# Kernel tuning notes

Hardware: AMD Instinct MI355X
Metric: run time of the kernel (lower is better)

## Reference

```python
import jax, jax.numpy as jnp
import numpy as np

N_NODES = 100000
N_EDGES = 1600000
IN_DIM = 128
HIDDEN = 128
N_GRAPHS = 256


def setup_inputs() -> dict:
    key = jax.random.key(0)
    ks = jax.random.split(key, 12)
    x = jax.random.normal(ks[0], (N_NODES, IN_DIM), dtype=jnp.float32)
    edge_index = jax.random.randint(ks[1], (2, N_EDGES), 0, N_NODES, dtype=jnp.int64)
    batch = jnp.sort(jax.random.randint(ks[2], (N_NODES,), 0, N_GRAPHS, dtype=jnp.int64))
    s = 0.05
    W1 = jax.random.normal(ks[3], (IN_DIM, HIDDEN), dtype=jnp.float32) * s
    b1 = jnp.zeros((HIDDEN,), dtype=jnp.float32)
    W2 = jax.random.normal(ks[4], (HIDDEN, HIDDEN), dtype=jnp.float32) * s
    b2 = jnp.zeros((HIDDEN,), dtype=jnp.float32)
    W3 = jax.random.normal(ks[5], (HIDDEN, HIDDEN), dtype=jnp.float32) * s
    b3 = jnp.zeros((HIDDEN,), dtype=jnp.float32)
    Wh = jax.random.normal(ks[6], (HIDDEN, 2), dtype=jnp.float32) * s
    bh = jnp.zeros((2,), dtype=jnp.float32)
    return {"x": x, "edge_index": edge_index, "batch": batch,
            "W1": W1, "b1": b1, "W2": W2, "b2": b2, "W3": W3, "b3": b3,
            "Wh": Wh, "bh": bh}


def _gcn_structure(edge_index, n_nodes):
    # PyG GCNConv default: add self-loops, symmetric deg^-1/2 normalization.
    loop = jnp.arange(n_nodes, dtype=edge_index.dtype)
    src = jnp.concatenate([edge_index[0], loop])  # message source j
    dst = jnp.concatenate([edge_index[1], loop])  # aggregate at i
    deg = jax.ops.segment_sum(jnp.ones_like(dst, dtype=jnp.float32), dst,
                              num_segments=n_nodes)
    dinv = jnp.where(deg > 0, jax.lax.rsqrt(deg), 0.0)
    norm = dinv[src] * dinv[dst]  # [E + N]
    return src, dst, norm


def _gcn_conv(x, W, b, src, dst, norm, n_nodes):
    h = x @ W  # dense transform first (PyG order)
    msg = h[src] * norm[:, None]  # gather + per-edge scale
    agg = jax.ops.segment_sum(msg, dst, num_segments=n_nodes)  # scatter-add
    return agg + b


def reference(x, edge_index, batch, W1, b1, W2, b2, W3, b3, Wh, bh):
    n = x.shape[0]
    src, dst, norm = _gcn_structure(edge_index, n)
    # dropout is a no-op in eval mode (training=False)
    h = jax.nn.relu(_gcn_conv(x, W1, b1, src, dst, norm, n))
    h = jax.nn.relu(_gcn_conv(h, W2, b2, src, dst, norm, n))
    h = jax.nn.relu(_gcn_conv(h, W3, b3, src, dst, norm, n))
    # global_mean_pool over graph ids
    sums = jax.ops.segment_sum(h, batch, num_segments=N_GRAPHS)
    cnts = jax.ops.segment_sum(jnp.ones((n,), dtype=h.dtype), batch,
                               num_segments=N_GRAPHS)
    pooled = sums / jnp.maximum(cnts, 1.0)[:, None]
    return pooled @ Wh + bh  # [N_GRAPHS, 2]
```

## Files before the change

kernel.cpp:

```cpp
#include <hip/hip_runtime.h>


#define D 128
#define NB_SHIFT 8
#define BCAP 8192
#define EPB 4096

typedef unsigned int uint;
typedef unsigned short ushort;
typedef __attribute__((ext_vector_type(8))) short short8;
typedef __attribute__((ext_vector_type(4))) float f32x4;

__device__ __forceinline__ ushort f2bf(float f) {
    uint u = __float_as_uint(f);
    uint r = (u + 0x7fffu + ((u >> 16) & 1u)) >> 16;
    return (ushort)r;
}
__device__ __forceinline__ float bf2f(ushort b) {
    return __uint_as_float(((uint)b) << 16);
}
__device__ __forceinline__ float q15f(uint q) {
    return __uint_as_float(0x30000000u | (q << 13));
}

__device__ __forceinline__ void async_cp16(const ushort* g, ushort* lds_uniform) {
    __builtin_amdgcn_global_load_lds(
        (const __attribute__((address_space(1))) unsigned int*)g,
        (__attribute__((address_space(3))) unsigned int*)lds_uniform,
        16, 0, 0);
}

__device__ __forceinline__ void bucketA_body(const int* __restrict__ src,
                                             const int* __restrict__ dst, int E,
                                             int nbk, int* __restrict__ gcur,
                                             uint* __restrict__ arena, int bid,
                                             int* hist, int* rbase) {
    int t = threadIdx.x;
    int e0 = bid * EPB;
    int e1 = min(e0 + EPB, E);
    for (int i = t; i < nbk; i += 256) hist[i] = 0;
    __syncthreads();
    for (int e = e0 + t; e < e1; e += 256)
        atomicAdd(&hist[dst[e] >> NB_SHIFT], 1);
    __syncthreads();
    for (int i = t; i < nbk; i += 256) {
        int c = hist[i];
        rbase[i] = (c > 0) ? atomicAdd(&gcur[i], c) : 0;
        hist[i] = 0;
    }
    __syncthreads();
    for (int e = e0 + t; e < e1; e += 256) {
        int d = dst[e];
        int s = src[e];
        int b = d >> NB_SHIFT;
        int pos = rbase[b] + atomicAdd(&hist[b], 1);
        if (pos < BCAP)
            arena[(size_t)b * BCAP + pos] =
                ((uint)(d & ((1 << NB_SHIFT) - 1)) << 17) | (uint)s;
    }
}

template <bool AF32>
__device__ __forceinline__ void gemm_body(const void* __restrict__ Ain,
                                          const ushort* __restrict__ Wf,
                                          ushort* __restrict__ out, int N,
                                          int rowb, ushort* As) {
    int t = threadIdx.x;

    if (AF32) {
        const float* A = (const float*)Ain;
#pragma unroll
        for (int i = 0; i < 8; i++) {
            int u = i * 256 + t;
            int row = u >> 5, c4 = u & 31;
            int grow = rowb + row;
            float4 v = make_float4(0.f, 0.f, 0.f, 0.f);
            if (grow < N) v = *(const float4*)(A + (size_t)grow * D + c4 * 4);
            uint2 p;
            p.x = (uint)f2bf(v.x) | ((uint)f2bf(v.y) << 16);
            p.y = (uint)f2bf(v.z) | ((uint)f2bf(v.w) << 16);
            int byteoff = row * 256 + ((c4 * 8) ^ ((row & 7) << 4));
            *(uint2*)((char*)As + byteoff) = p;
        }
    } else {
        const ushort* A = (const ushort*)Ain;
#pragma unroll
        for (int i = 0; i < 4; i++) {
            int u = i * 256 + t;
            int row = u >> 4, cp = u & 15;
            int grow = rowb + row;
            if (grow >= N) grow = N - 1;
            int gc = cp ^ (row & 7);
            const ushort* gp = A + (size_t)grow * D + gc * 8;
            ushort* lb = As + (size_t)(i * 256 + (t & 192)) * 8;
            async_cp16(gp, lb);
        }
        asm volatile("s_waitcnt vmcnt(0)" ::: "memory");
    }
    __syncthreads();

    int wave = t >> 6, lane = t & 63;
    const short8* Wf8 = (const short8*)Wf;

    short8 bhi[2][4], blo[2][4];
#pragma unroll
    for (int j = 0; j < 2; j++) {
        int nt = wave * 2 + j;
#pragma unroll
        for (int kt = 0; kt < 4; kt++) {
            bhi[j][kt] = Wf8[(size_t)((0 * 4 + kt) * 8 + nt) * 64 + lane];
            blo[j][kt] = Wf8[(size_t)((1 * 4 + kt) * 8 + nt) * 64 + lane];
        }
    }

    f32x4 acc[4][2];
#pragma unroll
    for (int m = 0; m < 4; m++)
#pragma unroll
        for (int j = 0; j < 2; j++) acc[m][j] = (f32x4){0.f, 0.f, 0.f, 0.f};

#pragma unroll
    for (int m = 0; m < 4; m++) {
        int r = m * 16 + (lane & 15);
#pragma unroll
        for (int kt = 0; kt < 4; kt++) {
            int raw = kt * 64 + (lane >> 4) * 16;
            short8 a = *(const short8*)((const char*)As + r * 256 + (raw ^ ((r & 7) << 4)));
#pragma unroll
            for (int j = 0; j < 2; j++) {
                acc[m][j] = __builtin_amdgcn_mfma_f32_16x16x32_bf16(a, bhi[j][kt], acc[m][j], 0, 0, 0);
                acc[m][j] = __builtin_amdgcn_mfma_f32_16x16x32_bf16(a, blo[j][kt], acc[m][j], 0, 0, 0);
            }
        }
    }

#pragma unroll
    for (int m = 0; m < 4; m++) {
#pragma unroll
        for (int j = 0; j < 2; j++) {
            int colb = (wave * 2 + j) * 16 + (lane & 15);
#pragma unroll
            for (int jj = 0; jj < 4; jj++) {
                int grow = rowb + m * 16 + (lane >> 4) * 4 + jj;
                if (grow < N)
                    out[(size_t)grow * D + colb] = f2bf(acc[m][j][jj]);
            }
        }
    }
}

__global__ __launch_bounds__(256) void k_build_gemm1(const int* __restrict__ src,
                                                     const int* __restrict__ dst, int E,
                                                     int nbk, int* __restrict__ gcur,
                                                     uint* __restrict__ arena, int nA,
                                                     const float* __restrict__ x,
                                                     const ushort* __restrict__ Wf,
                                                     ushort* __restrict__ T, int N) {
    __shared__ ushort As[64 * D];
    if ((int)blockIdx.x < nA) {
        int* hist = (int*)As;
        int* rbase = hist + 512;
        bucketA_body(src, dst, E, nbk, gcur, arena, blockIdx.x, hist, rbase);
    } else {
        gemm_body<true>(x, Wf, T, N, (blockIdx.x - nA) * 64, As);
    }
}

template <bool AF32>
__global__ __launch_bounds__(256) void k_gemm(const void* __restrict__ Ain,
                                              const ushort* __restrict__ Wf,
                                              ushort* __restrict__ out, int N) {
    __shared__ ushort As[64 * D];
    gemm_body<AF32>(Ain, Wf, out, N, blockIdx.x * 64, As);
}

__global__ void k_scanG(const int* __restrict__ gcur, int nbk, int E,
                        int* __restrict__ bbase, int* __restrict__ row_start, int N) {
    __shared__ int s[512];
    int t = threadIdx.x;
    s[t] = (t < nbk) ? gcur[t] : 0;
    __syncthreads();
    for (int off = 1; off < 512; off <<= 1) {
        int x = (t >= off) ? s[t - off] : 0;
        __syncthreads();
        s[t] += x;
        __syncthreads();
    }
    if (t < nbk) bbase[t] = s[t] - gcur[t];
    if (t == 0) row_start[N] = E;
}

__global__ __launch_bounds__(256) void k_degB2(const uint* __restrict__ arena,
                                               const int* __restrict__ gcur,
                                               const int* __restrict__ bbase, int N,
                                               float* __restrict__ dinv,
                                               int* __restrict__ row_start) {
    int b = blockIdx.x;
    int t = threadIdx.x;
    __shared__ int hist[256];
    __shared__ int sc[256];
    hist[t] = 0;
    __syncthreads();
    int cnt = min(gcur[b], BCAP);
    const uint* seg = arena + (size_t)b * BCAP;
    for (int i = t; i < cnt; i += 256)
        atomicAdd(&hist[seg[i] >> 17], 1);
    __syncthreads();
    int c = hist[t];
    sc[t] = c;
    __syncthreads();
    for (int off = 1; off < 256; off <<= 1) {
        int x = (t >= off) ? sc[t - off] : 0;
        __syncthreads();
        sc[t] += x;
        __syncthreads();
    }
    int node = (b << NB_SHIFT) + t;
    if (node < N) {
        dinv[node] = rsqrtf((float)(c + 1));
        row_start[node] = bbase[b] + sc[t] - c;
    }
}

__global__ __launch_bounds__(256) void k_bucketB(const uint* __restrict__ arena,
                                                 const int* __restrict__ gcur,
                                                 const int* __restrict__ row_start,
                                                 const float* __restrict__ dinv,
                                                 int N, uint* __restrict__ csr) {
    int b = blockIdx.x;
    int t = threadIdx.x;
    int n0 = b << NB_SHIFT;
    int nn = min(1 << NB_SHIFT, N - n0);
    __shared__ float sdinv[256];
    __shared__ int sstart[256];
    __shared__ int scur[256];
    __shared__ uint sout[BCAP];
    for (int i = t; i < nn; i += 256) {
        sdinv[i]  = dinv[n0 + i];
        sstart[i] = row_start[n0 + i];
        scur[i]   = 0;
    }
    __syncthreads();
    int cnt = min(gcur[b], BCAP);
    int csr0 = sstart[0];
    for (int i = t; i < cnt; i += 256) {
        uint en = arena[(size_t)b * BCAP + i];
        int dl = en >> 17;
        int s  = en & 0x1FFFF;
        float nrm = dinv[s] * sdinv[dl];
        uint q = ((__float_as_uint(nrm) + 0x1000u) >> 13) & 0x7FFFu;
        int pos = atomicAdd(&scur[dl], 1);
        sout[(sstart[dl] - csr0) + pos] = ((uint)s << 15) | q;
    }
    __syncthreads();
    for (int i = t; i < cnt; i += 256)
        csr[csr0 + i] = sout[i];
}

__global__ void k_wsplit3(const float* __restrict__ W1, const float* __restrict__ W2,
                          const float* __restrict__ W3, ushort* __restrict__ Wf) {
    int gidx = blockIdx.x * blockDim.x + threadIdx.x;
    if (gidx >= 3 * 32768) return;
    int which = gidx >> 15;
    int idx = gidx & 32767;
    const float* W = (which == 0) ? W1 : (which == 1) ? W2 : W3;
    int i  = idx & 7;
    int l  = (idx >> 3) & 63;
    int nt = (idx >> 9) & 7;
    int kt = (idx >> 12) & 3;
    int h  = idx >> 14;
    int k = kt * 32 + (l >> 4) * 8 + i;
    int n = nt * 16 + (l & 15);
    float w = W[k * D + n];
    ushort hi = f2bf(w);
    ushort v = (h == 0) ? hi : f2bf(w - bf2f(hi));
    Wf[gidx] = v;
}

__device__ __forceinline__ void agg_core(const ushort* __restrict__ T,
                                         const uint* __restrict__ csr,
                                         int beg, int end, int col,
                                         float& a0, float& a1) {
    if (beg >= end) return;
    int lane16 = threadIdx.x & 15;
    uint cur = csr[min(beg + lane16, end - 1)];
    for (int e = beg; e < end; e += 16) {
        uint nxt = 0;
        int en = e + 16;
        if (en < end) nxt = csr[min(en + lane16, end - 1)];
        uint v[16];
        float nn[16];
#pragma unroll
        for (int q = 0; q < 16; q++) {
            uint c = __builtin_amdgcn_readlane(cur, q);
            nn[q] = (e + q < end) ? q15f(c & 0x7FFFu) : 0.f;
            v[q] = *(const uint*)(T + (size_t)(c >> 15) * D + col);
        }
#pragma unroll
        for (int q = 0; q < 16; q++) {
            a0 = fmaf(nn[q], __uint_as_float(v[q] << 16), a0);
            a1 = fmaf(nn[q], __uint_as_float(v[q] & 0xffff0000u), a1);
        }
        cur = nxt;
    }
}

__global__ __launch_bounds__(256) void k_agg(const ushort* __restrict__ T,
                                             const float* __restrict__ dinv,
                                             const int* __restrict__ row_start,
                                             const uint* __restrict__ csr,
                                             const float* __restrict__ bias,
                                             ushort* __restrict__ out, int N) {
    int node = __builtin_amdgcn_readfirstlane(blockIdx.x * 4 + (threadIdx.x >> 6));
    if (node >= N) return;
    int lane = threadIdx.x & 63;
    int col = lane * 2;

    float di = dinv[node];
    uint vs = *(const uint*)(T + (size_t)node * D + col);
    float sw = di * di;
    float a0 = sw * __uint_as_float(vs << 16);
    float a1 = sw * __uint_as_float(vs & 0xffff0000u);

    agg_core(T, csr, row_start[node], row_start[node + 1], col, a0, a1);

    a0 = fmaxf(a0 + bias[col], 0.f);
    a1 = fmaxf(a1 + bias[col + 1], 0.f);
    ushort2 o; o.x = f2bf(a0); o.y = f2bf(a1);
    *(ushort2*)(out + (size_t)node * D + col) = o;
}

__global__ __launch_bounds__(256) void k_agg_head(const ushort* __restrict__ T,
                                                  const float* __restrict__ dinv,
                                                  const int* __restrict__ row_start,
                                                  const uint* __restrict__ csr,
                                                  const float* __restrict__ bias,
                                                  const float* __restrict__ Wh,
                                                  float2* __restrict__ y, int N) {
    int node = __builtin_amdgcn_readfirstlane(blockIdx.x * 4 + (threadIdx.x >> 6));
    if (node >= N) return;
    int lane = threadIdx.x & 63;
    int col = lane * 2;

    float di = dinv[node];
    uint vs = *(const uint*)(T + (size_t)node * D + col);
    float sw = di * di;
    float a0 = sw * __uint_as_float(vs << 16);
    float a1 = sw * __uint_as_float(vs & 0xffff0000u);

    agg_core(T, csr, row_start[node], row_start[node + 1], col, a0, a1);

    a0 = fmaxf(a0 + bias[col], 0.f);
    a1 = fmaxf(a1 + bias[col + 1], 0.f);

    float p0 = a0 * Wh[col * 2 + 0] + a1 * Wh[(col + 1) * 2 + 0];
    float p1 = a0 * Wh[col * 2 + 1] + a1 * Wh[(col + 1) * 2 + 1];
#pragma unroll
    for (int off = 32; off > 0; off >>= 1) {
        p0 += __shfl_xor(p0, off);
        p1 += __shfl_xor(p1, off);
    }
    if (lane == 0) y[node] = make_float2(p0, p1);
}

__global__ __launch_bounds__(256) void k_pool2(const float2* __restrict__ y,
                                               const int* __restrict__ batch, int N,
                                               const float* __restrict__ bh,
                                               float* __restrict__ out) {
    int g = blockIdx.x;
    int t = threadIdx.x;
    int lo = 0, hi = N;
    while (lo < hi) { int m = (lo + hi) >> 1; if (batch[m] < g) lo = m + 1; else hi = m; }
    int beg = lo;
    lo = 0; hi = N;
    while (lo < hi) { int m = (lo + hi) >> 1; if (batch[m] < g + 1) lo = m + 1; else hi = m; }
    int endi = lo;

    float s0 = 0.f, s1 = 0.f;
    for (int i = beg + t; i < endi; i += 256) {
        float2 v = y[i];
        s0 += v.x; s1 += v.y;
    }
    __shared__ float r0[256], r1[256];
    r0[t] = s0; r1[t] = s1;
    __syncthreads();
    for (int off = 128; off > 0; off >>= 1) {
        if (t < off) { r0[t] += r0[t + off]; r1[t] += r1[t + off]; }
        __syncthreads();
    }
    if (t == 0) {
        float cnt = (float)((endi - beg) > 0 ? (endi - beg) : 1);
        out[g * 2 + 0] = r0[0] / cnt + bh[0];
        out[g * 2 + 1] = r1[0] / cnt + bh[1];
    }
}

extern "C" void kernel_launch(void* const* d_in, const int* in_sizes, int n_in,
                              void* d_out, int out_size, void* d_ws, size_t ws_size,
                              hipStream_t stream) {
    const float* x   = (const float*)d_in[0];
    const int* eidx  = (const int*)d_in[1];
    const int* batch = (const int*)d_in[2];
    const float* W1 = (const float*)d_in[3];
    const float* b1 = (const float*)d_in[4];
    const float* W2 = (const float*)d_in[5];
    const float* b2 = (const float*)d_in[6];
    const float* W3 = (const float*)d_in[7];
    const float* b3 = (const float*)d_in[8];
    const float* Wh = (const float*)d_in[9];
    const float* bh = (const float*)d_in[10];

    int E = in_sizes[1] / 2;
    int N = in_sizes[2];
    int ngraphs = out_size / 2;
    const int* src = eidx;
    const int* dst = eidx + E;
    int nbk = (N + (1 << NB_SHIFT) - 1) >> NB_SHIFT;

    char* ws = (char*)d_ws;
    size_t off = 0;
    auto alloc = [&](size_t bytes) -> void* {
        void* p = ws + off;
        off = (off + bytes + 255) & ~(size_t)255;
        return p;
    };
    ushort* Hbf      = (ushort*)alloc((size_t)N * D * 2);
    ushort* T        = (ushort*)alloc((size_t)N * D * 2);
    ushort* Wf       = (ushort*)alloc(3 * 32768 * 2);
    float*  dinv     = (float*)alloc((size_t)N * 4);
    int*    row_start= (int*)alloc((size_t)(N + 1) * 4);
    int*    gcur     = (int*)alloc((size_t)nbk * 4);
    int*    bbase    = (int*)alloc((size_t)nbk * 4);
    float2* y        = (float2*)alloc((size_t)N * 8);
    uint*   csr      = (uint*)alloc((size_t)E * 4);
    uint*   arena    = (uint*)alloc((size_t)nbk * BCAP * 4);
    (void)ws_size;

    hipMemsetAsync(gcur, 0, (size_t)nbk * 4, stream);
    k_wsplit3<<<384, 256, 0, stream>>>(W1, W2, W3, Wf);

    int gemm_grid = (N + 63) / 64;
    int agg_grid = (N + 3) / 4;
    int nA = (E + EPB - 1) / EPB;

    k_build_gemm1<<<nA + gemm_grid, 256, 0, stream>>>(src, dst, E, nbk, gcur, arena,
                                                      nA, x, Wf, T, N);
    k_scanG<<<1, 512, 0, stream>>>(gcur, nbk, E, bbase, row_start, N);
    k_degB2<<<nbk, 256, 0, stream>>>(arena, gcur, bbase, N, dinv, row_start);
    k_bucketB<<<nbk, 256, 0, stream>>>(arena, gcur, row_start, dinv, N, csr);

    k_agg<<<agg_grid, 256, 0, stream>>>(T, dinv, row_start, csr, b1, Hbf, N);
    k_gemm<false><<<gemm_grid, 256, 0, stream>>>(Hbf, Wf + 32768, T, N);
    k_agg<<<agg_grid, 256, 0, stream>>>(T, dinv, row_start, csr, b2, Hbf, N);
    k_gemm<false><<<gemm_grid, 256, 0, stream>>>(Hbf, Wf + 65536, T, N);
    k_agg_head<<<agg_grid, 256, 0, stream>>>(T, dinv, row_start, csr, b3, Wh, y, N);
    k_pool2<<<ngraphs, 256, 0, stream>>>(y, batch, N, bh, (float*)d_out);
}
```

Before: 289.2 us.

## Fuse CSR build into one kernel and compute edge norms on the fly

```diff
diff --git a/kernel.cpp b/kernel.cpp
--- a/kernel.cpp
+++ b/kernel.cpp
@@ -18,9 +18,6 @@
 }
 __device__ __forceinline__ float bf2f(ushort b) {
     return __uint_as_float(((uint)b) << 16);
-}
-__device__ __forceinline__ float q15f(uint q) {
-    return __uint_as_float(0x30000000u | (q << 13));
 }
 
 __device__ __forceinline__ void async_cp16(const ushort* g, ushort* lds_uniform) {
@@ -174,92 +171,72 @@
     gemm_body<AF32>(Ain, Wf, out, N, blockIdx.x * 64, As);
 }
 
-__global__ void k_scanG(const int* __restrict__ gcur, int nbk, int E,
-                        int* __restrict__ bbase, int* __restrict__ row_start, int N) {
-    __shared__ int s[512];
-    int t = threadIdx.x;
-    s[t] = (t < nbk) ? gcur[t] : 0;
-    __syncthreads();
-    for (int off = 1; off < 512; off <<= 1) {
-        int x = (t >= off) ? s[t - off] : 0;
-        __syncthreads();
-        s[t] += x;
-        __syncthreads();
-    }
-    if (t < nbk) bbase[t] = s[t] - gcur[t];
-    if (t == 0) row_start[N] = E;
-}
-
-__global__ __launch_bounds__(256) void k_degB2(const uint* __restrict__ arena,
-                                               const int* __restrict__ gcur,
-                                               const int* __restrict__ bbase, int N,
-                                               float* __restrict__ dinv,
-                                               int* __restrict__ row_start) {
+__global__ __launch_bounds__(256) void k_bucketB2(const uint* __restrict__ arena,
+                                                  const int* __restrict__ gcur,
+                                                  int nbk, int N, int E,
+                                                  float* __restrict__ dinv,
+                                                  int* __restrict__ row_start,
+                                                  uint* __restrict__ csr) {
     int b = blockIdx.x;
     int t = threadIdx.x;
     __shared__ int hist[256];
     __shared__ int sc[256];
+    __shared__ uint sout[BCAP];
     hist[t] = 0;
     __syncthreads();
     int cnt = min(gcur[b], BCAP);
     const uint* seg = arena + (size_t)b * BCAP;
     for (int i = t; i < cnt; i += 256)
         atomicAdd(&hist[seg[i] >> 17], 1);
-    __syncthreads();
+
+    int p = 0;
+    if (t < b) p += gcur[t];
+    if (t + 256 < b) p += gcur[t + 256];
+    ((int*)sout)[t] = p;
+    __syncthreads();
+    for (int off2 = 128; off2 > 0; off2 >>= 1) {
+        if (t < off2) ((int*)sout)[t] += ((int*)sout)[t + off2];
+        __syncthreads();
+    }
+    int bbase = ((int*)sout)[0];
+
     int c = hist[t];
     sc[t] = c;
     __syncthreads();
-    for (int off = 1; off < 256; off <<= 1) {
-        int x = (t >= off) ? sc[t - off] : 0;
+    for (int off2 = 1; off2 < 256; off2 <<= 1) {
+        int x = (t >= off2) ? sc[t - off2] : 0;
         __syncthreads();
         sc[t] += x;
         __syncthreads();
     }
+    int excl = sc[t] - c;
+
     int node = (b << NB_SHIFT) + t;
     if (node < N) {
         dinv[node] = rsqrtf((float)(c + 1));
-        row_start[node] = bbase[b] + sc[t] - c;
-    }
-}
-
-__global__ __launch_bounds__(256) void k_bucketB(const uint* __restrict__ arena,
-                                                 const int* __restrict__ gcur,
-                                                 const int* __restrict__ row_start,
-                                                 const float* __restrict__ dinv,
-                                                 int N, uint* __restrict__ csr) {
-    int b = blockIdx.x;
-    int t = threadIdx.x;
-    int n0 = b << NB_SHIFT;
-    int nn = min(1 << NB_SHIFT, N - n0);
-    __shared__ float sdinv[256];
-    __shared__ int sstart[256];
-    __shared__ int scur[256];
-    __shared__ uint sout[BCAP];
-    for (int i = t; i < nn; i += 256) {
-        sdinv[i]  = dinv[n0 + i];
-        sstart[i] = row_start[n0 + i];
-        scur[i]   = 0;
-    }
-    __syncthreads();
-    int cnt = min(gcur[b], BCAP);
-    int csr0 = sstart[0];
+        row_start[node] = bbase + excl;
+    }
+    if (b == 0 && t == 0) row_start[N] = E;
+
+    sc[t] = excl;
+    hist[t] = 0;
+    __syncthreads();
     for (int i = t; i < cnt; i += 256) {
-        uint en = arena[(size_t)b * BCAP + i];
+        uint en = seg[i];
         int dl = en >> 17;
-        int s  = en & 0x1FFFF;
-        float nrm = dinv[s] * sdinv[dl];
-        uint q = ((__float_as_uint(nrm) + 0x1000u) >> 13) & 0x7FFFu;
-        int pos = atomicAdd(&scur[dl], 1);
-        sout[(sstart[dl] - csr0) + pos] = ((uint)s << 15) | q;
+        int pos = atomicAdd(&hist[dl], 1);
+        sout[sc[dl] + pos] = en & 0x1FFFF;
     }
     __syncthreads();
     for (int i = t; i < cnt; i += 256)
-        csr[csr0 + i] = sout[i];
+        csr[bbase + i] = sout[i];
 }
 
 __global__ void k_wsplit3(const float* __restrict__ W1, const float* __restrict__ W2,
-                          const float* __restrict__ W3, ushort* __restrict__ Wf) {
+                          const float* __restrict__ W3, ushort* __restrict__ Wf,
+                          int* __restrict__ gcur, int nbk) {
     int gidx = blockIdx.x * blockDim.x + threadIdx.x;
+    if (gidx < nbk) gcur[gidx] = 0;
     if (gidx >= 3 * 32768) return;
     int which = gidx >> 15;
     int idx = gidx & 32767;
@@ -279,7 +256,8 @@
 
 __device__ __forceinline__ void agg_core(const ushort* __restrict__ T,
                                          const uint* __restrict__ csr,
-                                         int beg, int end, int col,
+                                         const float* __restrict__ dinv,
+                                         float di, int beg, int end, int col,
                                          float& a0, float& a1) {
     if (beg >= end) return;
     int lane16 = threadIdx.x & 15;
@@ -293,8 +271,9 @@
 #pragma unroll
         for (int q = 0; q < 16; q++) {
             uint c = __builtin_amdgcn_readlane(cur, q);
-            nn[q] = (e + q < end) ? q15f(c & 0x7FFFu) : 0.f;
-            v[q] = *(const uint*)(T + (size_t)(c >> 15) * D + col);
+            float ds = dinv[c];
+            nn[q] = (e + q < end) ? ds * di : 0.f;
+            v[q] = *(const uint*)(T + (size_t)c * D + col);
         }
 #pragma unroll
         for (int q = 0; q < 16; q++) {
@@ -322,7 +301,7 @@
     float a0 = sw * __uint_as_float(vs << 16);
     float a1 = sw * __uint_as_float(vs & 0xffff0000u);
 
-    agg_core(T, csr, row_start[node], row_start[node + 1], col, a0, a1);
+    agg_core(T, csr, dinv, di, row_start[node], row_start[node + 1], col, a0, a1);
 
     a0 = fmaxf(a0 + bias[col], 0.f);
     a1 = fmaxf(a1 + bias[col + 1], 0.f);
@@ -348,7 +327,7 @@
     float a0 = sw * __uint_as_float(vs << 16);
     float a1 = sw * __uint_as_float(vs & 0xffff0000u);
 
-    agg_core(T, csr, row_start[node], row_start[node + 1], col, a0, a1);
+    agg_core(T, csr, dinv, di, row_start[node], row_start[node + 1], col, a0, a1);
 
     a0 = fmaxf(a0 + bias[col], 0.f);
     a1 = fmaxf(a1 + bias[col + 1], 0.f);
@@ -430,14 +409,12 @@
     float*  dinv     = (float*)alloc((size_t)N * 4);
     int*    row_start= (int*)alloc((size_t)(N + 1) * 4);
     int*    gcur     = (int*)alloc((size_t)nbk * 4);
-    int*    bbase    = (int*)alloc((size_t)nbk * 4);
     float2* y        = (float2*)alloc((size_t)N * 8);
     uint*   csr      = (uint*)alloc((size_t)E * 4);
     uint*   arena    = (uint*)alloc((size_t)nbk * BCAP * 4);
     (void)ws_size;
 
-    hipMemsetAsync(gcur, 0, (size_t)nbk * 4, stream);
-    k_wsplit3<<<384, 256, 0, stream>>>(W1, W2, W3, Wf);
+    k_wsplit3<<<384, 256, 0, stream>>>(W1, W2, W3, Wf, gcur, nbk);
 
     int gemm_grid = (N + 63) / 64;
     int agg_grid = (N + 3) / 4;
@@ -445,9 +422,7 @@
 
     k_build_gemm1<<<nA + gemm_grid, 256, 0, stream>>>(src, dst, E, nbk, gcur, arena,
                                                       nA, x, Wf, T, N);
-    k_scanG<<<1, 512, 0, stream>>>(gcur, nbk, E, bbase, row_start, N);
-    k_degB2<<<nbk, 256, 0, stream>>>(arena, gcur, bbase, N, dinv, row_start);
-    k_bucketB<<<nbk, 256, 0, stream>>>(arena, gcur, row_start, dinv, N, csr);
+    k_bucketB2<<<nbk, 256, 0, stream>>>(arena, gcur, nbk, N, E, dinv, row_start, csr);
 
     k_agg<<<agg_grid, 256, 0, stream>>>(T, dinv, row_start, csr, b1, Hbf, N);
     k_gemm<false><<<gemm_grid, 256, 0, stream>>>(Hbf, Wf + 32768, T, N);
```

Measured after the change: 321.7 us. 1.11x slower.
